# Optimization experiments

Hardware: AMD Instinct MI355X
Metric: run time of the kernel (lower is better)

## Reference

```python
import jax, jax.numpy as jnp
import numpy as np

DIM = 256
HEADS = 8
DIM_HEAD = 64
INNER = HEADS * DIM_HEAD  # 512
SCALE = DIM_HEAD ** -0.5
EPS = 1e-5


def _layernorm(x, w, b):
    mu = jnp.mean(x, axis=-1, keepdims=True)
    var = jnp.var(x, axis=-1, keepdims=True)
    return (x - mu) * jax.lax.rsqrt(var + EPS) * w + b


def setup_inputs() -> dict:
    key = jax.random.key(0)
    ks = jax.random.split(key, 20)
    B, N, M, H, W = 8, 4096, 256, 64, 64
    s = 0.02
    inp = {
        "feat": jax.random.normal(ks[0], (B, N, DIM), jnp.float32),
        "center": jax.random.normal(ks[1], (B, M, DIM), jnp.float32),
        "pos": jax.random.normal(ks[2], (B, DIM, H, W), jnp.float32),
        "center_pos": jax.random.normal(ks[3], (B, M, DIM), jnp.float32),
        # projection weights stored [in, out] so y = x @ W
        "Wq": jax.random.normal(ks[4], (DIM, INNER), jnp.float32) * s,
        "Wk": jax.random.normal(ks[5], (DIM, INNER), jnp.float32) * s,
        "Wv1": jax.random.normal(ks[6], (DIM, INNER), jnp.float32) * s,
        "Wv2": jax.random.normal(ks[7], (DIM, INNER), jnp.float32) * s,
        "Wo1": jax.random.normal(ks[8], (INNER, DIM), jnp.float32) * s,
        "Wo2": jax.random.normal(ks[9], (INNER, DIM), jnp.float32) * s,
        "ln1_w": jnp.ones((DIM,), jnp.float32),
        "ln1_b": jnp.zeros((DIM,), jnp.float32),
        "ln2_w": jnp.ones((DIM,), jnp.float32),
        "ln2_b": jnp.zeros((DIM,), jnp.float32),
        "ffn1_W1": jax.random.normal(ks[10], (DIM, DIM), jnp.float32) * s,
        "ffn1_W2": jax.random.normal(ks[11], (DIM, DIM), jnp.float32) * s,
        "ffn1_b2": jnp.zeros((DIM,), jnp.float32),
        "ffn2_W1": jax.random.normal(ks[12], (DIM, DIM), jnp.float32) * s,
        "ffn2_W2": jax.random.normal(ks[13], (DIM, DIM), jnp.float32) * s,
        "ffn2_b2": jnp.zeros((DIM,), jnp.float32),
    }
    return inp


def reference(feat, center, pos, center_pos, Wq, Wk, Wv1, Wv2, Wo1, Wo2,
              ln1_w, ln1_b, ln2_w, ln2_b, ffn1_W1, ffn1_W2, ffn1_b2,
              ffn2_W1, ffn2_W2, ffn2_b2):
    B = feat.shape[0]
    # pos: [B, C, H, W] -> [B, N, C]
    pos_f = pos.reshape(B, DIM, -1).transpose(0, 2, 1)
    q = (feat + pos_f) @ Wq            # [B, N, INNER]
    k = (center + center_pos) @ Wk     # [B, M, INNER]
    v1 = feat @ Wv1                    # [B, N, INNER]
    v2 = center @ Wv2                  # [B, M, INNER]

    def split(x):  # [B, T, h*d] -> [B, h, T, d]
        return x.reshape(B, x.shape[1], HEADS, DIM_HEAD).transpose(0, 2, 1, 3)

    q, k, v1, v2 = split(q), split(k), split(v1), split(v2)
    attn = jnp.einsum("bhnd,bhmd->bhnm", q, k) * SCALE  # [B, h, N, M]
    attn1 = jax.nn.softmax(attn, axis=-2)  # over N (queries)
    attn2 = jax.nn.softmax(attn, axis=-1)  # over M (keys)
    out_feat = jnp.einsum("bhnm,bhmd->bhnd", attn2, v2)    # [B, h, N, d]
    out_center = jnp.einsum("bhnm,bhnd->bhmd", attn1, v1)  # [B, h, M, d]

    def merge(x):  # [B, h, T, d] -> [B, T, h*d]
        return x.transpose(0, 2, 1, 3).reshape(B, x.shape[2], INNER)

    out_feat = merge(out_feat) @ Wo1 + feat
    out_center = merge(out_center) @ Wo2 + center
    out_feat = _layernorm(out_feat, ln1_w, ln1_b)
    out_center = _layernorm(out_center, ln2_w, ln2_b)
    out_feat = jax.nn.relu(out_feat @ ffn1_W1) @ ffn1_W2 + ffn1_b2 + out_feat
    out_center = jax.nn.relu(out_center @ ffn2_W1) @ ffn2_W2 + ffn2_b2 + out_center
    return out_feat, out_center
```

## Files before the change

kernel.cpp:

```cpp
#include <hip/hip_runtime.h>

typedef __bf16 bf16;
typedef __bf16 bf16x4 __attribute__((ext_vector_type(4)));
typedef __bf16 bf16x8 __attribute__((ext_vector_type(8)));
typedef float f32x4 __attribute__((ext_vector_type(4)));

#define MFMA16(a, b, c) __builtin_amdgcn_mfma_f32_16x16x32_bf16(a, b, c, 0, 0, 0)

#define CEXP 0.18033688011112042f

struct WTArgs {
  const float* src[10];
  bf16* dst[10];
  int K[10];
  int N[10];
};

__global__ __launch_bounds__(256) void wtrans_kernel(WTArgs args) {
  const int z = blockIdx.z;
  const int K = args.K[z], N = args.N[z];
  const int k0 = blockIdx.x * 64, n0 = blockIdx.y * 64;
  if (k0 >= K || n0 >= N) return;
  __shared__ float t[64][65];
  const int tx = threadIdx.x & 63, ty = threadIdx.x >> 6;
  const float* __restrict__ src = args.src[z];
  bf16* __restrict__ dst = args.dst[z];
#pragma unroll
  for (int i = 0; i < 16; ++i)
    t[ty + i * 4][tx] = src[(size_t)(k0 + ty + i * 4) * N + n0 + tx];
  __syncthreads();
#pragma unroll
  for (int i = 0; i < 16; ++i)
    dst[(size_t)(n0 + ty + i * 4) * K + k0 + tx] = (bf16)t[tx][ty + i * 4];
}

__global__ __launch_bounds__(256) void prep_xq_kernel(
    const float* __restrict__ feat, const float* __restrict__ pos,
    bf16* __restrict__ xq) {
  const int n0 = blockIdx.x * 64;
  const int c0 = blockIdx.y * 64;
  const int b = blockIdx.z;
  __shared__ float t[64][65];
  const int tx = threadIdx.x & 63, ty = threadIdx.x >> 6;
#pragma unroll
  for (int i = 0; i < 16; ++i) {
    int c = ty + i * 4;
    t[c][tx] = pos[((size_t)b * 256 + c0 + c) * 4096 + n0 + tx];
  }
  __syncthreads();
#pragma unroll
  for (int i = 0; i < 16; ++i) {
    int n = ty + i * 4;
    size_t off = ((size_t)b * 4096 + n0 + n) * 256 + c0 + tx;
    xq[off] = (bf16)(feat[off] + t[tx][n]);
  }
}

__device__ inline void stage16(const bf16* g, bf16* l) {
  __builtin_amdgcn_global_load_lds(
      (const __attribute__((address_space(1))) void*)g,
      (__attribute__((address_space(3))) void*)l, 16, 0, 0);
}
__device__ inline void stage16(const float* g, bf16* l) {
  f32x4 u = *(const f32x4*)g;
  f32x4 v = *((const f32x4*)g + 1);
  bf16x8 o;
#pragma unroll
  for (int i = 0; i < 4; ++i) {
    o[i] = (bf16)u[i];
    o[4 + i] = (bf16)v[i];
  }
  *(bf16x8*)l = o;
}
__device__ inline void stage16(const float* g, const float* g2, bf16* l) {
  f32x4 u = *(const f32x4*)g + *(const f32x4*)g2;
  f32x4 v = *((const f32x4*)g + 1) + *((const f32x4*)g2 + 1);
  bf16x8 o;
#pragma unroll
  for (int i = 0; i < 4; ++i) {
    o[i] = (bf16)u[i];
    o[4 + i] = (bf16)v[i];
  }
  *(bf16x8*)l = o;
}

__device__ inline f32x4 rload(const float* p) { return *(const f32x4*)p; }
__device__ inline f32x4 rload(const bf16* p) {
  bf16x4 t = *(const bf16x4*)p;
  return (f32x4){(float)t[0], (float)t[1], (float)t[2], (float)t[3]};
}
__device__ inline void cstore(float* p, f32x4 v) { *(f32x4*)p = v; }
__device__ inline void cstore(bf16* p, f32x4 v) {
  bf16x4 o;
  o[0] = (bf16)v[0]; o[1] = (bf16)v[1]; o[2] = (bf16)v[2]; o[3] = (bf16)v[3];
  *(bf16x4*)p = o;
}

struct GArg {
  const void* A[2];
  const void* A2[2];
  const bf16* BT[2];
  void* C[2];
  const void* resid[2];
  const float* bias[2];
  int M[2];
};

template <int EPI, typename TO, typename TR, typename TA, bool FUSE2>
__global__ __launch_bounds__(256) void gemm_kernel(GArg g, int N, int K) {
  const int z = blockIdx.z;
  const int m0 = blockIdx.x * 128;
  if (m0 >= g.M[z]) return;
  const TA* A = (const TA*)g.A[z];
  const TA* A2 = (const TA*)g.A2[z];
  const bf16* BT = g.BT[z];
  TO* C = (TO*)g.C[z];
  const TR* resid = (const TR*)g.resid[z];
  const float* bias = g.bias[z];

  const int n0 = blockIdx.y * 128;
  const int tid = threadIdx.x;
  const int lane = tid & 63;
  const int w = tid >> 6;
  const int wr = (w >> 1) * 64, wc = (w & 1) * 64;
  const int l15 = lane & 15, quad = lane >> 4;

  __shared__ __align__(16) bf16 Al[2][128 * 32];
  __shared__ __align__(16) bf16 Bl[2][128 * 32];

  f32x4 acc[4][4];
#pragma unroll
  for (int i = 0; i < 4; ++i)
#pragma unroll
    for (int j = 0; j < 4; ++j) acc[i][j] = (f32x4){0.f, 0.f, 0.f, 0.f};

  const int sw = (((l15 >> 1) & 3) ^ quad) * 8;

  auto stage = [&](int buf, int k0) {
#pragma unroll
    for (int c = 0; c < 2; ++c) {
      int idx = tid + c * 256;
      int row = idx >> 2;
      int gs = ((idx & 3) ^ ((row >> 1) & 3)) * 8;
      size_t aoff = (size_t)(m0 + row) * K + k0 + gs;
      if constexpr (FUSE2)
        stage16(A + aoff, A2 + aoff, Al[buf] + idx * 8);
      else
        stage16(A + aoff, Al[buf] + idx * 8);
      stage16(BT + (size_t)(n0 + row) * K + k0 + gs, Bl[buf] + idx * 8);
    }
  };

  stage(0, 0);
  int cur = 0;
  const int nt = K >> 5;
  for (int t = 0; t < nt; ++t) {
    __syncthreads();
    if (t + 1 < nt) stage(cur ^ 1, (t + 1) * 32);
    bf16x8 fa[4], fb[4];
#pragma unroll
    for (int i = 0; i < 4; ++i) {
      fa[i] = *(const bf16x8*)(Al[cur] + (wr + i * 16 + l15) * 32 + sw);
      fb[i] = *(const bf16x8*)(Bl[cur] + (wc + i * 16 + l15) * 32 + sw);
    }
#pragma unroll
    for (int i = 0; i < 4; ++i)
#pragma unroll
      for (int j = 0; j < 4; ++j)
        acc[i][j] = MFMA16(fb[j], fa[i], acc[i][j]);
    cur ^= 1;
  }

#pragma unroll
  for (int i = 0; i < 4; ++i) {
#pragma unroll
    for (int j = 0; j < 4; ++j) {
      int row = m0 + wr + i * 16 + l15;
      int col = n0 + wc + j * 16 + quad * 4;
      size_t off = (size_t)row * N + col;
      f32x4 v = acc[i][j];
      if constexpr (EPI == 1) {
#pragma unroll
        for (int e = 0; e < 4; ++e) v[e] = fmaxf(v[e], 0.f);
      }
      if constexpr (EPI == 2) v += rload(resid + off);
      if constexpr (EPI == 3)
        v += rload(resid + off) + *(const f32x4*)(bias + col);
      cstore(C + off, v);
    }
  }
}

__global__ __launch_bounds__(256, 1) void attf_kernel(
    const bf16* q, const bf16* __restrict__ kk, const bf16* __restrict__ v1,
    const bf16* __restrict__ v2, bf16* af, float* __restrict__ acc_p,
    float* __restrict__ colsum_p) {
  const int nb = blockIdx.x;
  const int h = blockIdx.y;
  const int b = blockIdx.z;
  const int tid = threadIdx.x;
  const int lane = tid & 63;
  const int w = tid >> 6;
  const int l15 = lane & 15, quad = lane >> 4;

  __shared__ __align__(16) bf16 klds[256 * 72];
  __shared__ __align__(16) bf16 v2T[64 * 264];
  __shared__ __align__(16) bf16 v1T[2][64 * 72];
  __shared__ __align__(16) bf16 PT[256 * 72];

#pragma unroll
  for (int c = 0; c < 8; ++c) {
    int idx = tid + c * 256;
    int m = idx >> 3;
    int dc = (idx & 7) * 8;
    *(bf16x8*)(klds + m * 72 + dc) =
        *(const bf16x8*)(kk + ((size_t)(b * 256 + m)) * 512 + h * 64 + dc);
  }
#pragma unroll
  for (int c = 0; c < 8; ++c) {
    int idx = tid + c * 256;
    int m = idx >> 3;
    int dc = (idx & 7) * 8;
    bf16x8 t =
        *(const bf16x8*)(v2 + ((size_t)(b * 256 + m)) * 512 + h * 64 + dc);
    int p = (m & ~31) |
            (((((m >> 2) & 3) << 3) + (m & 3)) + (((m >> 4) & 1) << 2));
#pragma unroll
    for (int j = 0; j < 8; ++j) v2T[(dc + j) * 264 + p] = t[j];
  }
  {
    const int nl = tid >> 3;
    const int dc = (tid & 7) * 8;
    const bf16* v1b =
        v1 + ((size_t)(b * 4096 + nb * 1024)) * 512 + h * 64 + dc;
    bf16x8 t0 = *(const bf16x8*)(v1b + (size_t)nl * 512);
    bf16x8 t1 = *(const bf16x8*)(v1b + (size_t)(nl + 32) * 512);
#pragma unroll
    for (int j = 0; j < 8; ++j) {
      v1T[0][(dc + j) * 72 + nl] = t0[j];
      v1T[0][(dc + j) * 72 + nl + 32] = t1[j];
    }
  }
  bf16x8 qa0, qa1;
  {
    int nrow = b * 4096 + nb * 1024 + w * 16 + l15;
    const bf16* qp = q + (size_t)nrow * 512 + h * 64 + quad * 8;
    qa0 = *(const bf16x8*)(qp);
    qa1 = *(const bf16x8*)(qp + 32);
  }

  f32x4 oc2[16];
#pragma unroll
  for (int i = 0; i < 16; ++i) oc2[i] = (f32x4){0.f, 0.f, 0.f, 0.f};
  f32x4 csa[4];
#pragma unroll
  for (int i = 0; i < 4; ++i) csa[i] = (f32x4){0.f, 0.f, 0.f, 0.f};
  bf16x8 ones8;
#pragma unroll
  for (int j = 0; j < 8; ++j) ones8[j] = (bf16)1.0f;

  __syncthreads();

  for (int ch = 0; ch < 16; ++ch) {
    bf16x8 v1a, v1b;
    const int nl = tid >> 3;
    const int dc = (tid & 7) * 8;
    if (ch < 15) {
      const bf16* v1p =
          v1 + ((size_t)(b * 4096 + nb * 1024 + (ch + 1) * 64)) * 512 +
          h * 64 + dc;
      v1a = *(const bf16x8*)(v1p + (size_t)nl * 512);
      v1b = *(const bf16x8*)(v1p + (size_t)(nl + 32) * 512);
    }

    bf16x8 pa[8];
    float rs = 0.f;
#pragma unroll
    for (int mt = 0; mt < 16; ++mt) {
      const bf16* kp = klds + (mt * 16 + l15) * 72 + quad * 8;
      bf16x8 ka0 = *(const bf16x8*)(kp);
      bf16x8 ka1 = *(const bf16x8*)(kp + 32);
      f32x4 s = (f32x4){0.f, 0.f, 0.f, 0.f};
      s = MFMA16(ka0, qa0, s);
      s = MFMA16(ka1, qa1, s);
      float e0 = exp2f(s[0] * CEXP);
      float e1 = exp2f(s[1] * CEXP);
      float e2 = exp2f(s[2] * CEXP);
      float e3 = exp2f(s[3] * CEXP);
      rs += (e0 + e1) + (e2 + e3);
      bf16 b0 = (bf16)e0, b1 = (bf16)e1, b2 = (bf16)e2, b3 = (bf16)e3;
      int mrow = mt * 16 + quad * 4;
      PT[(mrow + 0) * 72 + w * 16 + l15] = b0;
      PT[(mrow + 1) * 72 + w * 16 + l15] = b1;
      PT[(mrow + 2) * 72 + w * 16 + l15] = b2;
      PT[(mrow + 3) * 72 + w * 16 + l15] = b3;
      pa[mt >> 1][(mt & 1) * 4 + 0] = b0;
      pa[mt >> 1][(mt & 1) * 4 + 1] = b1;
      pa[mt >> 1][(mt & 1) * 4 + 2] = b2;
      pa[mt >> 1][(mt & 1) * 4 + 3] = b3;
    }

    f32x4 o1[4];
#pragma unroll
    for (int i = 0; i < 4; ++i) o1[i] = (f32x4){0.f, 0.f, 0.f, 0.f};
#pragma unroll
    for (int ks = 0; ks < 8; ++ks) {
#pragma unroll
      for (int dt = 0; dt < 4; ++dt) {
        bf16x8 vb = *(const bf16x8*)(v2T + (dt * 16 + l15) * 264 + ks * 32 +
                                     quad * 8);
        o1[dt] = MFMA16(vb, pa[ks], o1[dt]);
      }
    }
    {
      float rsf = rs + __shfl_xor(rs, 16, 64);
      rsf += __shfl_xor(rsf, 32, 64);
      float inv = 1.f / rsf;
      int n = nb * 1024 + ch * 64 + w * 16 + l15;
      bf16* ap = af + ((size_t)(b * 4096 + n)) * 512 + h * 64 + quad * 4;
#pragma unroll
      for (int dt = 0; dt < 4; ++dt) {
        bf16x4 ov;
        ov[0] = (bf16)(o1[dt][0] * inv);
        ov[1] = (bf16)(o1[dt][1] * inv);
        ov[2] = (bf16)(o1[dt][2] * inv);
        ov[3] = (bf16)(o1[dt][3] * inv);
        *(bf16x4*)(ap + dt * 16) = ov;
      }
    }

    if (ch < 15) {
      bf16* dst = v1T[(ch + 1) & 1];
#pragma unroll
      for (int j = 0; j < 8; ++j) {
        dst[(dc + j) * 72 + nl] = v1a[j];
        dst[(dc + j) * 72 + nl + 32] = v1b[j];
      }
    }
    __syncthreads();

    bf16x8 qn0 = qa0, qn1 = qa1;
    if (ch < 15) {
      int nrow = b * 4096 + nb * 1024 + (ch + 1) * 64 + w * 16 + l15;
      const bf16* qp = q + (size_t)nrow * 512 + h * 64 + quad * 8;
      qn0 = *(const bf16x8*)(qp);
      qn1 = *(const bf16x8*)(qp + 32);
    }

    const bf16* vc = v1T[ch & 1];
#pragma unroll
    for (int ks = 0; ks < 2; ++ks) {
      bf16x8 vbv[4];
#pragma unroll
      for (int dt = 0; dt < 4; ++dt)
        vbv[dt] = *(const bf16x8*)(vc + (dt * 16 + l15) * 72 + ks * 32 +
                                   quad * 8);
#pragma unroll
      for (int mq = 0; mq < 4; ++mq) {
        bf16x8 pa2 = *(const bf16x8*)(PT + (mq * 64 + w * 16 + l15) * 72 +
                                      ks * 32 + quad * 8);
#pragma unroll
        for (int dt = 0; dt < 4; ++dt)
          oc2[mq * 4 + dt] = MFMA16(vbv[dt], pa2, oc2[mq * 4 + dt]);
        csa[mq] = MFMA16(pa2, ones8, csa[mq]);
      }
    }
    __syncthreads();
    qa0 = qn0;
    qa1 = qn1;
  }

  const size_t slab = (size_t)(nb * 64 + b * 8 + h);
  if (l15 == 0) {
#pragma unroll
    for (int mq = 0; mq < 4; ++mq)
#pragma unroll
      for (int r = 0; r < 4; ++r)
        colsum_p[slab * 256 + mq * 64 + w * 16 + quad * 4 + r] = csa[mq][r];
  }
  float* base = acc_p + slab * (256 * 64);
#pragma unroll
  for (int mq = 0; mq < 4; ++mq) {
    int m = mq * 64 + w * 16 + l15;
#pragma unroll
    for (int dt = 0; dt < 4; ++dt)
      *(f32x4*)(base + m * 64 + dt * 16 + quad * 4) = oc2[mq * 4 + dt];
  }
}

__global__ __launch_bounds__(256) void acm_kernel(
    const float* __restrict__ acc_p, const float* __restrict__ colsum_p,
    bf16* __restrict__ acm) {
  int idx = blockIdx.x * 256 + threadIdx.x;
  int d = idx & 63;
  int h = (idx >> 6) & 7;
  int m = (idx >> 9) & 255;
  int b = idx >> 17;
  float cv = 0.f, v = 0.f;
#pragma unroll
  for (int p = 0; p < 4; ++p) {
    cv += colsum_p[((size_t)(p * 64 + b * 8 + h)) * 256 + m];
    v += acc_p[(((size_t)(p * 64 + b * 8 + h)) * 256 + m) * 64 + d];
  }
  acm[idx] = (bf16)(v / cv);
}

__global__ __launch_bounds__(256) void ln_kernel(
    const bf16* __restrict__ x0, const bf16* __restrict__ x1,
    const float* __restrict__ w0, const float* __restrict__ b0,
    const float* __restrict__ w1, const float* __restrict__ b1,
    bf16* __restrict__ y0, bf16* __restrict__ y1, int rows0, int rows1) {
  int wave = threadIdx.x >> 6;
  int lane = threadIdx.x & 63;
  int row = blockIdx.x * 4 + wave;
  const bf16* x;
  const float *wv, *bv;
  bf16* y;
  if (row < rows0) {
    x = x0; wv = w0; bv = b0; y = y0;
  } else {
    row -= rows0;
    if (row >= rows1) return;
    x = x1; wv = w1; bv = b1; y = y1;
  }
  const bf16* xr = x + (size_t)row * 256;
  bf16x4 v = *(const bf16x4*)(xr + lane * 4);
  float f0 = v[0], f1 = v[1], f2 = v[2], f3 = v[3];
  float s = f0 + f1 + f2 + f3;
  float ss = f0 * f0 + f1 * f1 + f2 * f2 + f3 * f3;
#pragma unroll
  for (int m = 1; m < 64; m <<= 1) {
    s += __shfl_xor(s, m, 64);
    ss += __shfl_xor(ss, m, 64);
  }
  float mean = s * (1.f / 256.f);
  float var = ss * (1.f / 256.f) - mean * mean;
  float rstd = rsqrtf(var + 1e-5f);
  f32x4 wq = *(const f32x4*)(wv + lane * 4);
  f32x4 bq = *(const f32x4*)(bv + lane * 4);
  bf16x4 o;
  o[0] = (bf16)((f0 - mean) * rstd * wq[0] + bq[0]);
  o[1] = (bf16)((f1 - mean) * rstd * wq[1] + bq[1]);
  o[2] = (bf16)((f2 - mean) * rstd * wq[2] + bq[2]);
  o[3] = (bf16)((f3 - mean) * rstd * wq[3] + bq[3]);
  *(bf16x4*)(y + (size_t)row * 256 + lane * 4) = o;
}

extern "C" void kernel_launch(void* const* d_in, const int* in_sizes, int n_in,
                              void* d_out, int out_size, void* d_ws,
                              size_t ws_size, hipStream_t stream) {
  const float* feat = (const float*)d_in[0];
  const float* center = (const float*)d_in[1];
  const float* pos = (const float*)d_in[2];
  const float* cpos = (const float*)d_in[3];
  const float* Wq = (const float*)d_in[4];
  const float* Wk = (const float*)d_in[5];
  const float* Wv1 = (const float*)d_in[6];
  const float* Wv2 = (const float*)d_in[7];
  const float* Wo1 = (const float*)d_in[8];
  const float* Wo2 = (const float*)d_in[9];
  const float* ln1w = (const float*)d_in[10];
  const float* ln1b = (const float*)d_in[11];
  const float* ln2w = (const float*)d_in[12];
  const float* ln2b = (const float*)d_in[13];
  const float* f1W1 = (const float*)d_in[14];
  const float* f1W2 = (const float*)d_in[15];
  const float* f1b2 = (const float*)d_in[16];
  const float* f2W1 = (const float*)d_in[17];
  const float* f2W2 = (const float*)d_in[18];
  const float* f2b2 = (const float*)d_in[19];

  char* ws = (char*)d_ws;
  const size_t MB = 1024 * 1024;
  bf16* q_ = (bf16*)(ws + 0);
  bf16* af_ = q_;
  bf16* v1_ = (bf16*)(ws + 32 * MB);
  bf16* xq_ = (bf16*)(ws + 64 * MB);
  float* accp_ = (float*)(ws + 64 * MB);
  bf16* rf_ = xq_;
  bf16* k_ = (bf16*)(ws + 80 * MB);
  bf16* rc_ = (bf16*)(ws + 82 * MB);
  bf16* v2_ = (bf16*)(ws + 83 * MB);
  bf16* acm_ = v2_;
  float* colsum_ = (float*)(ws + 89 * MB);
  bf16* wt_ = (bf16*)(ws + 89 * MB + 262144);
  bf16* yf_ = q_;
  bf16* tf_ = (bf16*)(ws + 16 * MB);
  bf16* yc_ = (bf16*)(ws + 92 * MB);
  bf16* tc_ = (bf16*)(ws + 93 * MB);

  bf16* WqT = wt_;
  bf16* WkT = WqT + 131072;
  bf16* Wv1T = WkT + 131072;
  bf16* Wv2T = Wv1T + 131072;
  bf16* Wo1T = Wv2T + 131072;
  bf16* Wo2T = Wo1T + 131072;
  bf16* f1W1T = Wo2T + 131072;
  bf16* f1W2T = f1W1T + 65536;
  bf16* f2W1T = f1W2T + 65536;
  bf16* f2W2T = f2W1T + 65536;

  float* out_feat = (float*)d_out;
  float* out_center = out_feat + (size_t)8 * 4096 * 256;

  WTArgs wa;
  const float* srcs[10] = {Wq, Wk, Wv1, Wv2, Wo1, Wo2, f1W1, f1W2, f2W1, f2W2};
  bf16* dsts[10] = {WqT, WkT, Wv1T, Wv2T, Wo1T, Wo2T, f1W1T, f1W2T, f2W1T, f2W2T};
  int Ks[10] = {256, 256, 256, 256, 512, 512, 256, 256, 256, 256};
  int Ns[10] = {512, 512, 512, 512, 256, 256, 256, 256, 256, 256};
  for (int i = 0; i < 10; ++i) {
    wa.src[i] = srcs[i];
    wa.dst[i] = dsts[i];
    wa.K[i] = Ks[i];
    wa.N[i] = Ns[i];
  }

  wtrans_kernel<<<dim3(8, 8, 10), 256, 0, stream>>>(wa);
  prep_xq_kernel<<<dim3(64, 4, 8), 256, 0, stream>>>(feat, pos, xq_);

  {
    GArg a{};
    a.A[0] = xq_; a.BT[0] = WqT; a.C[0] = q_; a.M[0] = 32768;
    gemm_kernel<0, bf16, bf16, bf16, false>
        <<<dim3(256, 4, 1), 256, 0, stream>>>(a, 512, 256);
  }
  {
    GArg a{};
    a.A[0] = center; a.A2[0] = cpos; a.BT[0] = WkT; a.C[0] = k_;
    a.M[0] = 2048;
    gemm_kernel<0, bf16, bf16, float, true>
        <<<dim3(16, 4, 1), 256, 0, stream>>>(a, 512, 256);
  }
  {
    GArg a{};
    a.A[0] = feat; a.A[1] = center;
    a.BT[0] = Wv1T; a.BT[1] = Wv2T;
    a.C[0] = v1_; a.C[1] = v2_;
    a.M[0] = 32768; a.M[1] = 2048;
    gemm_kernel<0, bf16, bf16, float, false>
        <<<dim3(256, 4, 2), 256, 0, stream>>>(a, 512, 256);
  }

  attf_kernel<<<dim3(4, 8, 8), 256, 0, stream>>>(q_, k_, v1_, v2_, af_, accp_,
                                                 colsum_);
  acm_kernel<<<dim3(4096), 256, 0, stream>>>(accp_, colsum_, acm_);

  {
    GArg a{};
    a.A[0] = af_; a.A[1] = acm_;
    a.BT[0] = Wo1T; a.BT[1] = Wo2T;
    a.C[0] = rf_; a.C[1] = rc_;
    a.resid[0] = feat; a.resid[1] = center;
    a.M[0] = 32768; a.M[1] = 2048;
    gemm_kernel<2, bf16, float, bf16, false>
        <<<dim3(256, 2, 2), 256, 0, stream>>>(a, 256, 512);
  }
  ln_kernel<<<dim3(8704), 256, 0, stream>>>(rf_, rc_, ln1w, ln1b, ln2w, ln2b,
                                            yf_, yc_, 32768, 2048);
  {
    GArg a{};
    a.A[0] = yf_; a.A[1] = yc_;
    a.BT[0] = f1W1T; a.BT[1] = f2W1T;
    a.C[0] = tf_; a.C[1] = tc_;
    a.M[0] = 32768; a.M[1] = 2048;
    gemm_kernel<1, bf16, bf16, bf16, false>
        <<<dim3(256, 2, 2), 256, 0, stream>>>(a, 256, 256);
  }
  {
    GArg a{};
    a.A[0] = tf_; a.A[1] = tc_;
    a.BT[0] = f1W2T; a.BT[1] = f2W2T;
    a.C[0] = out_feat; a.C[1] = out_center;
    a.resid[0] = yf_; a.resid[1] = yc_;
    a.bias[0] = f1b2; a.bias[1] = f2b2;
    a.M[0] = 32768; a.M[1] = 2048;
    gemm_kernel<3, float, bf16, bf16, false>
        <<<dim3(256, 2, 2), 256, 0, stream>>>(a, 256, 256);
  }
}
```

Measured before the change: 359.2 us.

## Fuse LayerNorm and both FFN GEMMs into one kernel; prefetch fp32 A tiles into registers

Replaces the separate layernorm kernel and the two FFN GEMM launches with one ffn_kernel. Each 128-row tile is normalized into LDS, multiplied through W1 with ReLU into LDS, then through W2 with bias and residual added before the fp32 output is written. This removes the global round trips for the normalized and hidden activations and two launches. In exchange it runs one large-LDS block per CU with 256 row tiles, and weight chunks are restaged through LDS with syncs. Separately, the generic GEMM now loads fp32 A operands into registers one iteration early and converts and writes them to LDS after the MFMAs, so the load latency overlaps with compute.

Result: slower. 371.3 us (+3.4%).

```diff
diff --git a/kernel.cpp b/kernel.cpp
--- a/kernel.cpp
+++ b/kernel.cpp
@@ -61,28 +61,6 @@
       (const __attribute__((address_space(1))) void*)g,
       (__attribute__((address_space(3))) void*)l, 16, 0, 0);
 }
-__device__ inline void stage16(const float* g, bf16* l) {
-  f32x4 u = *(const f32x4*)g;
-  f32x4 v = *((const f32x4*)g + 1);
-  bf16x8 o;
-#pragma unroll
-  for (int i = 0; i < 4; ++i) {
-    o[i] = (bf16)u[i];
-    o[4 + i] = (bf16)v[i];
-  }
-  *(bf16x8*)l = o;
-}
-__device__ inline void stage16(const float* g, const float* g2, bf16* l) {
-  f32x4 u = *(const f32x4*)g + *(const f32x4*)g2;
-  f32x4 v = *((const f32x4*)g + 1) + *((const f32x4*)g2 + 1);
-  bf16x8 o;
-#pragma unroll
-  for (int i = 0; i < 4; ++i) {
-    o[i] = (bf16)u[i];
-    o[4 + i] = (bf16)v[i];
-  }
-  *(bf16x8*)l = o;
-}
 
 __device__ inline f32x4 rload(const float* p) { return *(const f32x4*)p; }
 __device__ inline f32x4 rload(const bf16* p) {
@@ -111,6 +89,7 @@
   const int z = blockIdx.z;
   const int m0 = blockIdx.x * 128;
   if (m0 >= g.M[z]) return;
+  constexpr bool F32A = sizeof(TA) == 4;
   const TA* A = (const TA*)g.A[z];
   const TA* A2 = (const TA*)g.A2[z];
   const bf16* BT = g.BT[z];
@@ -136,27 +115,89 @@
 
   const int sw = (((l15 >> 1) & 3) ^ quad) * 8;
 
-  auto stage = [&](int buf, int k0) {
+  f32x4 ar[2][2], ar2[2][2];
+
+  auto stageB = [&](int buf, int k0) {
 #pragma unroll
     for (int c = 0; c < 2; ++c) {
       int idx = tid + c * 256;
       int row = idx >> 2;
       int gs = ((idx & 3) ^ ((row >> 1) & 3)) * 8;
-      size_t aoff = (size_t)(m0 + row) * K + k0 + gs;
-      if constexpr (FUSE2)
-        stage16(A + aoff, A2 + aoff, Al[buf] + idx * 8);
-      else
-        stage16(A + aoff, Al[buf] + idx * 8);
       stage16(BT + (size_t)(n0 + row) * K + k0 + gs, Bl[buf] + idx * 8);
     }
   };
-
-  stage(0, 0);
+  auto stageA_dma = [&](int buf, int k0) {
+    if constexpr (!F32A) {
+#pragma unroll
+      for (int c = 0; c < 2; ++c) {
+        int idx = tid + c * 256;
+        int row = idx >> 2;
+        int gs = ((idx & 3) ^ ((row >> 1) & 3)) * 8;
+        stage16((const bf16*)A + (size_t)(m0 + row) * K + k0 + gs,
+                Al[buf] + idx * 8);
+      }
+    }
+  };
+  auto loadA = [&](int k0) {
+    if constexpr (F32A) {
+      const float* Af = (const float*)(const void*)A;
+      const float* A2f = (const float*)(const void*)A2;
+#pragma unroll
+      for (int c = 0; c < 2; ++c) {
+        int idx = tid + c * 256;
+        int row = idx >> 2;
+        int gs = ((idx & 3) ^ ((row >> 1) & 3)) * 8;
+        const float* p = Af + (size_t)(m0 + row) * K + k0 + gs;
+        ar[c][0] = *(const f32x4*)p;
+        ar[c][1] = *((const f32x4*)p + 1);
+        if constexpr (FUSE2) {
+          const float* p2 = A2f + (size_t)(m0 + row) * K + k0 + gs;
+          ar2[c][0] = *(const f32x4*)p2;
+          ar2[c][1] = *((const f32x4*)p2 + 1);
+        }
+      }
+    }
+  };
+  auto writeA = [&](int buf) {
+    if constexpr (F32A) {
+#pragma unroll
+      for (int c = 0; c < 2; ++c) {
+        int idx = tid + c * 256;
+        f32x4 u = ar[c][0], v = ar[c][1];
+        if constexpr (FUSE2) {
+          u += ar2[c][0];
+          v += ar2[c][1];
+        }
+        bf16x8 o;
+#pragma unroll
+        for (int e = 0; e < 4; ++e) {
+          o[e] = (bf16)u[e];
+          o[4 + e] = (bf16)v[e];
+        }
+        *(bf16x8*)(Al[buf] + idx * 8) = o;
+      }
+    }
+  };
+
+  if constexpr (F32A) {
+    loadA(0);
+    writeA(0);
+  } else {
+    stageA_dma(0, 0);
+  }
+  stageB(0, 0);
+
   int cur = 0;
   const int nt = K >> 5;
   for (int t = 0; t < nt; ++t) {
     __syncthreads();
-    if (t + 1 < nt) stage(cur ^ 1, (t + 1) * 32);
+    if (t + 1 < nt) {
+      stageB(cur ^ 1, (t + 1) * 32);
+      if constexpr (F32A)
+        loadA((t + 1) * 32);
+      else
+        stageA_dma(cur ^ 1, (t + 1) * 32);
+    }
     bf16x8 fa[4], fb[4];
 #pragma unroll
     for (int i = 0; i < 4; ++i) {
@@ -168,6 +209,9 @@
 #pragma unroll
       for (int j = 0; j < 4; ++j)
         acc[i][j] = MFMA16(fb[j], fa[i], acc[i][j]);
+    if constexpr (F32A) {
+      if (t + 1 < nt) writeA(cur ^ 1);
+    }
     cur ^= 1;
   }
 
@@ -189,6 +233,140 @@
       cstore(C + off, v);
     }
   }
+}
+
+struct FArg {
+  const bf16* x[2];
+  const float* lnw[2];
+  const float* lnb[2];
+  const bf16* W1T[2];
+  const bf16* W2T[2];
+  const float* bias[2];
+  float* out[2];
+  int M[2];
+};
+
+__global__ __launch_bounds__(256, 1) void ffn_kernel(FArg g) {
+  const int z = blockIdx.z;
+  const int m0 = blockIdx.x * 128;
+  if (m0 >= g.M[z]) return;
+  const int tid = threadIdx.x;
+  const int lane = tid & 63;
+  const int w = tid >> 6;
+  const int l15 = lane & 15, quad = lane >> 4;
+
+  __shared__ __align__(16) bf16 Y[128 * 264];
+  __shared__ __align__(16) bf16 T[128 * 264];
+  __shared__ __align__(16) bf16 Wc[256 * 40];
+
+  {
+    const int row = tid >> 1, c0 = (tid & 1) * 128;
+    const bf16* xr = g.x[z] + (size_t)(m0 + row) * 256 + c0;
+    bf16x8 v[16];
+#pragma unroll
+    for (int i = 0; i < 16; ++i) v[i] = *(const bf16x8*)(xr + i * 8);
+    float s = 0.f, ss = 0.f;
+#pragma unroll
+    for (int i = 0; i < 16; ++i)
+#pragma unroll
+      for (int e = 0; e < 8; ++e) {
+        float f = (float)v[i][e];
+        s += f;
+        ss += f * f;
+      }
+    s += __shfl_xor(s, 1, 64);
+    ss += __shfl_xor(ss, 1, 64);
+    float mean = s * (1.f / 256.f);
+    float var = ss * (1.f / 256.f) - mean * mean;
+    float rstd = rsqrtf(var + 1e-5f);
+    const float* wv = g.lnw[z] + c0;
+    const float* bv = g.lnb[z] + c0;
+    bf16* yr = Y + row * 264 + c0;
+#pragma unroll
+    for (int i = 0; i < 16; ++i) {
+      f32x4 w0 = *(const f32x4*)(wv + i * 8);
+      f32x4 w1 = *(const f32x4*)(wv + i * 8 + 4);
+      f32x4 b0 = *(const f32x4*)(bv + i * 8);
+      f32x4 b1 = *(const f32x4*)(bv + i * 8 + 4);
+      bf16x8 o;
+#pragma unroll
+      for (int e = 0; e < 4; ++e) {
+        o[e] = (bf16)(((float)v[i][e] - mean) * rstd * w0[e] + b0[e]);
+        o[4 + e] = (bf16)(((float)v[i][4 + e] - mean) * rstd * w1[e] + b1[e]);
+      }
+      *(bf16x8*)(yr + i * 8) = o;
+    }
+  }
+  __syncthreads();
+
+  f32x4 acc[2][16];
+  auto run_gemm = [&](const bf16* SRC, const bf16* WT) {
+#pragma unroll
+    for (int i = 0; i < 2; ++i)
+#pragma unroll
+      for (int j = 0; j < 16; ++j) acc[i][j] = (f32x4){0.f, 0.f, 0.f, 0.f};
+    bf16x8 wrg[4];
+    {
+      const bf16* wp = WT + (size_t)tid * 256;
+#pragma unroll
+      for (int c = 0; c < 4; ++c) wrg[c] = *(const bf16x8*)(wp + c * 8);
+    }
+    for (int ks = 0; ks < 8; ++ks) {
+#pragma unroll
+      for (int c = 0; c < 4; ++c)
+        *(bf16x8*)(Wc + tid * 40 + c * 8) = wrg[c];
+      __syncthreads();
+      if (ks < 7) {
+        const bf16* wp = WT + (size_t)tid * 256 + (ks + 1) * 32;
+#pragma unroll
+        for (int c = 0; c < 4; ++c) wrg[c] = *(const bf16x8*)(wp + c * 8);
+      }
+      bf16x8 fa[2];
+#pragma unroll
+      for (int i = 0; i < 2; ++i)
+        fa[i] = *(const bf16x8*)(SRC + (w * 32 + i * 16 + l15) * 264 +
+                                 ks * 32 + quad * 8);
+#pragma unroll
+      for (int j = 0; j < 16; ++j) {
+        bf16x8 fb = *(const bf16x8*)(Wc + (j * 16 + l15) * 40 + quad * 8);
+#pragma unroll
+        for (int i = 0; i < 2; ++i) acc[i][j] = MFMA16(fb, fa[i], acc[i][j]);
+      }
+      __syncthreads();
+    }
+  };
+
+  run_gemm(Y, g.W1T[z]);
+#pragma unroll
+  for (int i = 0; i < 2; ++i)
+#pragma unroll
+    for (int j = 0; j < 16; ++j) {
+      int m = w * 32 + i * 16 + l15;
+      int n = j * 16 + quad * 4;
+      bf16x4 o;
+#pragma unroll
+      for (int e = 0; e < 4; ++e) o[e] = (bf16)fmaxf(acc[i][j][e], 0.f);
+      *(bf16x4*)(T + m * 264 + n) = o;
+    }
+  __syncthreads();
+
+  run_gemm(T, g.W2T[z]);
+  const float* bias = g.bias[z];
+  float* out = g.out[z];
+#pragma unroll
+  for (int i = 0; i < 2; ++i)
+#pragma unroll
+    for (int j = 0; j < 16; ++j) {
+      int m = w * 32 + i * 16 + l15;
+      int n = j * 16 + quad * 4;
+      bf16x4 yv = *(const bf16x4*)(Y + m * 264 + n);
+      f32x4 v = acc[i][j] + *(const f32x4*)(bias + n);
+      v[0] += (float)yv[0];
+      v[1] += (float)yv[1];
+      v[2] += (float)yv[2];
+      v[3] += (float)yv[3];
+      *(f32x4*)(out + (size_t)(m0 + m) * 256 + n) = v;
+    }
 }
 
 __global__ __launch_bounds__(256, 1) void attf_kernel(
@@ -403,47 +581,6 @@
     v += acc_p[(((size_t)(p * 64 + b * 8 + h)) * 256 + m) * 64 + d];
   }
   acm[idx] = (bf16)(v / cv);
-}
-
-__global__ __launch_bounds__(256) void ln_kernel(
-    const bf16* __restrict__ x0, const bf16* __restrict__ x1,
-    const float* __restrict__ w0, const float* __restrict__ b0,
-    const float* __restrict__ w1, const float* __restrict__ b1,
-    bf16* __restrict__ y0, bf16* __restrict__ y1, int rows0, int rows1) {
-  int wave = threadIdx.x >> 6;
-  int lane = threadIdx.x & 63;
-  int row = blockIdx.x * 4 + wave;
-  const bf16* x;
-  const float *wv, *bv;
-  bf16* y;
-  if (row < rows0) {
-    x = x0; wv = w0; bv = b0; y = y0;
-  } else {
-    row -= rows0;
-    if (row >= rows1) return;
-    x = x1; wv = w1; bv = b1; y = y1;
-  }
-  const bf16* xr = x + (size_t)row * 256;
-  bf16x4 v = *(const bf16x4*)(xr + lane * 4);
-  float f0 = v[0], f1 = v[1], f2 = v[2], f3 = v[3];
-  float s = f0 + f1 + f2 + f3;
-  float ss = f0 * f0 + f1 * f1 + f2 * f2 + f3 * f3;
-#pragma unroll
-  for (int m = 1; m < 64; m <<= 1) {
-    s += __shfl_xor(s, m, 64);
-    ss += __shfl_xor(ss, m, 64);
-  }
-  float mean = s * (1.f / 256.f);
-  float var = ss * (1.f / 256.f) - mean * mean;
-  float rstd = rsqrtf(var + 1e-5f);
-  f32x4 wq = *(const f32x4*)(wv + lane * 4);
-  f32x4 bq = *(const f32x4*)(bv + lane * 4);
-  bf16x4 o;
-  o[0] = (bf16)((f0 - mean) * rstd * wq[0] + bq[0]);
-  o[1] = (bf16)((f1 - mean) * rstd * wq[1] + bq[1]);
-  o[2] = (bf16)((f2 - mean) * rstd * wq[2] + bq[2]);
-  o[3] = (bf16)((f3 - mean) * rstd * wq[3] + bq[3]);
-  *(bf16x4*)(y + (size_t)row * 256 + lane * 4) = o;
 }
 
 extern "C" void kernel_launch(void* const* d_in, const int* in_sizes, int n_in,
@@ -484,10 +621,6 @@
   bf16* acm_ = v2_;
   float* colsum_ = (float*)(ws + 89 * MB);
   bf16* wt_ = (bf16*)(ws + 89 * MB + 262144);
-  bf16* yf_ = q_;
-  bf16* tf_ = (bf16*)(ws + 16 * MB);
-  bf16* yc_ = (bf16*)(ws + 92 * MB);
-  bf16* tc_ = (bf16*)(ws + 93 * MB);
 
   bf16* WqT = wt_;
   bf16* WkT = WqT + 131072;
@@ -555,26 +688,16 @@
     gemm_kernel<2, bf16, float, bf16, false>
         <<<dim3(256, 2, 2), 256, 0, stream>>>(a, 256, 512);
   }
-  ln_kernel<<<dim3(8704), 256, 0, stream>>>(rf_, rc_, ln1w, ln1b, ln2w, ln2b,
-                                            yf_, yc_, 32768, 2048);
   {
-    GArg a{};
-    a.A[0] = yf_; a.A[1] = yc_;
-    a.BT[0] = f1W1T; a.BT[1] = f2W1T;
-    a.C[0] = tf_; a.C[1] = tc_;
-    a.M[0] = 32768; a.M[1] = 2048;
-    gemm_kernel<1, bf16, bf16, bf16, false>
-        <<<dim3(256, 2, 2), 256, 0, stream>>>(a, 256, 256);
-  }
-  {
-    GArg a{};
-    a.A[0] = tf_; a.A[1] = tc_;
-    a.BT[0] = f1W2T; a.BT[1] = f2W2T;
-    a.C[0] = out_feat; a.C[1] = out_center;
-    a.resid[0] = yf_; a.resid[1] = yc_;
-    a.bias[0] = f1b2; a.bias[1] = f2b2;
-    a.M[0] = 32768; a.M[1] = 2048;
-    gemm_kernel<3, float, bf16, bf16, false>
-        <<<dim3(256, 2, 2), 256, 0, stream>>>(a, 256, 256);
-  }
-}
+    FArg f{};
+    f.x[0] = rf_; f.x[1] = rc_;
+    f.lnw[0] = ln1w; f.lnb[0] = ln1b;
+    f.lnw[1] = ln2w; f.lnb[1] = ln2b;
+    f.W1T[0] = f1W1T; f.W1T[1] = f2W1T;
+    f.W2T[0] = f1W2T; f.W2T[1] = f2W2T;
+    f.bias[0] = f1b2; f.bias[1] = f2b2;
+    f.out[0] = out_feat; f.out[1] = out_center;
+    f.M[0] = 32768; f.M[1] = 2048;
+    ffn_kernel<<<dim3(256, 1, 2), 256, 0, stream>>>(f);
+  }
+}
```
